# Kernel tuning notes

Hardware: AMD Instinct MI355X
Metric: run time of the kernel (lower is better)

## Reference

```python
import jax, jax.numpy as jnp
import numpy as np

DIM = 256
NUM_HEADS = 8
NUM_NEI = (16, 32)
G = len(NUM_NEI)          # branches
G_H = NUM_HEADS // G      # heads per branch = 4
G_DIM = DIM // G          # channels per branch = 128
HD = G_DIM // G_H         # head dim = 32
SCALE = HD ** (-0.5)
M_MSF = G                 # MSF branches
CHANNEL = DIM // M_MSF    # 128
D_MSF = CHANNEL           # r=1

gelu = lambda t: jax.nn.gelu(t, approximate=False)


def setup_inputs() -> dict:
    key = jax.random.key(0)
    ks = jax.random.split(key, 16)
    B, N = 4, 2048
    s = lambda fan: fan ** (-0.5)
    inp = {
        "x": jax.random.normal(ks[0], (B, N, DIM), jnp.float32),
        "pos": jax.random.uniform(ks[1], (B, N, 3), jnp.float32),
        # qkv linear (no bias); stored as (in, out)
        "Wqkv": jax.random.normal(ks[2], (DIM, 3 * DIM), jnp.float32) * s(DIM),
        # per-branch rel-pos MLPs: Linear(3, g_dim) + GELU
        "Wp0": jax.random.normal(ks[3], (3, G_DIM), jnp.float32) * s(3),
        "bp0": jnp.zeros((G_DIM,), jnp.float32),
        "Wp1": jax.random.normal(ks[4], (3, G_DIM), jnp.float32) * s(3),
        "bp1": jnp.zeros((G_DIM,), jnp.float32),
        # MSF params
        "W_proj": jax.random.normal(ks[5], (DIM, DIM), jnp.float32) * s(DIM),
        "b_proj": jnp.zeros((DIM,), jnp.float32),
        "W_fc1": jax.random.normal(ks[6], (DIM, D_MSF), jnp.float32) * s(DIM),
        "b_fc1": jnp.zeros((D_MSF,), jnp.float32),
        "W_fc2": jax.random.normal(ks[7], (D_MSF, M_MSF * CHANNEL), jnp.float32) * s(D_MSF),
        "b_fc2": jnp.zeros((M_MSF * CHANNEL,), jnp.float32),
        "W_head": jax.random.normal(ks[8], (DIM, DIM), jnp.float32) * s(DIM),
        "b_head": jnp.zeros((DIM,), jnp.float32),
    }
    return inp


def _branch(q, k, v, pos, knn_idx, Wp, bp):
    """One head-group: KNN gather + rel-pos MLP fused attention.
    q,k,v: [B,N,g_dim]; pos: [B,N,3]; knn_idx: [B,N,nk]."""
    B, N, g_dim = k.shape
    nk = knn_idx.shape[-1]
    gather = jax.vmap(lambda t, idx: t[idx])  # per-batch fancy gather -> [B,N,nk,D]
    knn_xyz = gather(pos, knn_idx)                       # [B,N,nk,3]
    kg = gather(k, knn_idx)                              # [B,N,nk,g_dim]
    vg = gather(v, knn_idx)
    # split heads: b n k (h d) -> b h n k d
    split = lambda t: t.reshape(B, N, nk, G_H, HD).transpose(0, 3, 1, 2, 4)
    kg, vg = split(kg), split(vg)
    rel = pos[:, :, None, :] - knn_xyz                   # [B,N,nk,3]
    vrp = split(gelu(rel @ Wp + bp))                     # [B,h,N,nk,d]
    vg = vg + vrp
    attn_rel = vrp.sum(-1)                               # [B,h,N,nk]
    qh = q.reshape(B, N, G_H, HD).transpose(0, 2, 1, 3)  # [B,h,N,d]
    logits = jnp.einsum('bhnd,bhnkd->bhnk', qh, kg) * SCALE + attn_rel
    a = jax.nn.softmax(logits, axis=-1)
    out = jnp.einsum('bhnk,bhnkd->bhnd', a, vg)          # [B,h,N,d]
    return out.transpose(0, 2, 1, 3).reshape(B, N, g_dim)


def _msf(x, W_proj, b_proj, W_fc1, b_fc1, W_fc2, b_fc2, W_head, b_head):
    bs, N, dim = x.shape
    input_groups = x.transpose(0, 2, 1).reshape(bs, M_MSF, CHANNEL, N)
    feats_proj = gelu(x @ W_proj + b_proj)               # [bs,N,dim]
    feats_S = feats_proj.mean(axis=1)                    # global avg pool over N -> [bs,dim]
    feats_Z = gelu(feats_S @ W_fc1 + b_fc1)
    av = (feats_Z @ W_fc2 + b_fc2).reshape(bs, M_MSF, CHANNEL, 1)
    av = jax.nn.softmax(av, axis=1)                      # softmax over branches
    feats_V = (input_groups * av).reshape(bs, dim, N).transpose(0, 2, 1)
    feats_V = feats_V @ W_head + b_head
    return feats_proj + feats_V


def reference(x, pos, Wqkv, Wp0, bp0, Wp1, bp1,
              W_proj, b_proj, W_fc1, b_fc1, W_fc2, b_fc2, W_head, b_head):
    B, N, C = x.shape
    # pairwise squared distances [B,N,N] (broadcast form, as in source)
    dists = jnp.sum((pos[:, :, None, :] - pos[:, None, :, :]) ** 2, axis=-1)
    order = jnp.argsort(dists, axis=-1)                  # [B,N,N]
    qkv = (x @ Wqkv).reshape(B, N, 3, C).transpose(2, 0, 1, 3)  # [3,B,N,C]
    pos_params = [(Wp0, bp0), (Wp1, bp1)]
    outs = []
    for i, nk in enumerate(NUM_NEI):
        sl = slice(i * G_DIM, (i + 1) * G_DIM)
        q, k, v = qkv[0][..., sl], qkv[1][..., sl], qkv[2][..., sl]
        knn_idx = order[:, :, :nk]
        Wp, bp = pos_params[i]
        outs.append(_branch(q, k, v, pos, knn_idx, Wp, bp))
    xcat = jnp.concatenate(outs, axis=-1)                # [B,N,C]
    return _msf(xcat, W_proj, b_proj, W_fc1, b_fc1, W_fc2, b_fc2, W_head, b_head)
```

## Files before the change

kernel.cpp:

```cpp
#include <hip/hip_runtime.h>
#include <cstdint>
#include <cstddef>

#define B_    4
#define NPT   2048
#define DIM_  256
#define QKVW  768
#define XLEN  2097152
#define QLEN  196608
#define PLEN  65536
#define TOTC  (XLEN + QLEN + 2 * PLEN)

typedef unsigned short ushort_t;
typedef unsigned long long u64;
typedef short bf16x8 __attribute__((ext_vector_type(8)));
typedef float f32x4 __attribute__((ext_vector_type(4)));

__device__ __forceinline__ float gelu_f(float x) {
  return 0.5f * x * (1.0f + erff(x * 0.70710678118654752440f));
}

__device__ __forceinline__ float gelu_fast(float x) {
  const float is2 = 0.70710678118654752440f;
  float z = x * is2;
  float az = __builtin_fabsf(z);
  float t = __builtin_amdgcn_rcpf(fmaf(0.3275911f, az, 1.0f));
  float p = fmaf(1.061405429f, t, -1.453152027f);
  p = fmaf(p, t, 1.421413741f);
  p = fmaf(p, t, -0.284496736f);
  p = fmaf(p, t, 0.254829592f);
  p = p * t;
  float e = __expf(-az * az);
  float er = fmaf(-p, e, 1.0f);
  er = __builtin_copysignf(er, x);
  return 0.5f * x * (1.0f + er);
}

__device__ __forceinline__ ushort_t f2bf(float f) {
  unsigned u = __float_as_uint(f);
  unsigned r = (u + 0x7fffu + ((u >> 16) & 1u)) >> 16;
  return (ushort_t)r;
}
__device__ __forceinline__ float bf2f(ushort_t h) {
  return __uint_as_float(((unsigned)h) << 16);
}

template <int CTRL>
__device__ __forceinline__ float dpp_addf(float x) {
  int s = __builtin_amdgcn_update_dpp(0, __float_as_int(x), CTRL, 0xf, 0xf, false);
  return x + __int_as_float(s);
}
template <int CTRL>
__device__ __forceinline__ int dpp_addi(int x) {
  int s = __builtin_amdgcn_update_dpp(0, x, CTRL, 0xf, 0xf, false);
  return x + s;
}
__device__ __forceinline__ float head32_reduce(float u) {
  u = dpp_addf<0x111>(u);
  u = dpp_addf<0x112>(u);
  u = dpp_addf<0x114>(u);
  u = dpp_addf<0x118>(u);
  u = dpp_addf<0x142>(u);
  return u;
}
__device__ __forceinline__ int wave_sum_i(int x) {
  x = dpp_addi<0x111>(x);
  x = dpp_addi<0x112>(x);
  x = dpp_addi<0x114>(x);
  x = dpp_addi<0x118>(x);
  x = dpp_addi<0x142>(x);
  x = dpp_addi<0x143>(x);
  return x;
}

__device__ __forceinline__ bf16x8 scale_bf(bf16x8 v, const float* avk) {
  bf16x8 r;
#pragma unroll
  for (int e = 0; e < 8; e++) {
    float f = bf2f((ushort_t)v[e]) * avk[e];
    r[e] = (short)f2bf(f);
  }
  return r;
}

__global__ __launch_bounds__(256) void convert_kernel(
    const float* __restrict__ x, const float* __restrict__ Wqkv,
    const float* __restrict__ Wproj, const float* __restrict__ Whead,
    ushort_t* __restrict__ xbf, ushort_t* __restrict__ WqkvT,
    ushort_t* __restrict__ WprojT, ushort_t* __restrict__ WheadT,
    float* __restrict__ part) {
  int base = blockIdx.x * 256 + threadIdx.x;
  if (base < 1024) part[base] = 0.f;
  for (int i = base; i < TOTC; i += 2048 * 256) {
    if (i < XLEN) {
      xbf[i] = f2bf(x[i]);
    } else if (i < XLEN + QLEN) {
      int e = i - XLEN;
      int k = e / 768, n = e - k * 768;
      WqkvT[n * 256 + k] = f2bf(Wqkv[e]);
    } else if (i < XLEN + QLEN + PLEN) {
      int e = i - XLEN - QLEN;
      int k = e >> 8, n = e & 255;
      WprojT[n * 256 + k] = f2bf(Wproj[e]);
    } else {
      int e = i - XLEN - QLEN - PLEN;
      int k = e >> 8, n = e & 255;
      WheadT[n * 256 + k] = f2bf(Whead[e]);
    }
  }
}

__global__ __launch_bounds__(64, 4) void knn_gemm0_kernel(
    const float* __restrict__ pos, int* __restrict__ idx_out,
    const ushort_t* __restrict__ A, const ushort_t* __restrict__ BT,
    float* __restrict__ C) {
  __shared__ u64 buf[128];
  __shared__ unsigned cnt;
  int lane = threadIdx.x;
  if (blockIdx.x >= 8192) {
    constexpr int K = 256;
    constexpr int N = 768;
    int quad = lane >> 4, r16 = lane & 15;
    int t0 = blockIdx.x - 8192;
    int m0 = (t0 / 24) * 64, n0 = (t0 % 24) * 32;
    const ushort_t* Ap = A + (size_t)(m0 + r16) * K + quad * 8;
    const ushort_t* Bp = BT + (size_t)(n0 + r16) * K + quad * 8;
    f32x4 acc[4][2] = {};
    bf16x8 af[4], bfv[2], af2[4], bf2[2];
#pragma unroll
    for (int i = 0; i < 4; i++) af[i] = *(const bf16x8*)(Ap + (size_t)i * 16 * K);
#pragma unroll
    for (int j = 0; j < 2; j++) bfv[j] = *(const bf16x8*)(Bp + (size_t)j * 16 * K);
#pragma unroll
    for (int kc = 0; kc < 8; kc++) {
      if (kc < 7) {
        int ko = (kc + 1) * 32;
#pragma unroll
        for (int i = 0; i < 4; i++)
          af2[i] = *(const bf16x8*)(Ap + (size_t)i * 16 * K + ko);
#pragma unroll
        for (int j = 0; j < 2; j++)
          bf2[j] = *(const bf16x8*)(Bp + (size_t)j * 16 * K + ko);
      }
#pragma unroll
      for (int i = 0; i < 4; i++) {
        acc[i][0] = __builtin_amdgcn_mfma_f32_16x16x32_bf16(af[i], bfv[0], acc[i][0], 0, 0, 0);
        acc[i][1] = __builtin_amdgcn_mfma_f32_16x16x32_bf16(af[i], bfv[1], acc[i][1], 0, 0, 0);
      }
#pragma unroll
      for (int i = 0; i < 4; i++) af[i] = af2[i];
      bfv[0] = bf2[0]; bfv[1] = bf2[1];
    }
#pragma unroll
    for (int i = 0; i < 4; i++) {
#pragma unroll
      for (int j = 0; j < 2; j++) {
        int col = n0 + j * 16 + r16;
#pragma unroll
        for (int r = 0; r < 4; r++) {
          int row = m0 + i * 16 + quad * 4 + r;
          C[(size_t)row * N + col] = acc[i][j][r];
        }
      }
    }
    return;
  }
  int wq = blockIdx.x;
  int b = wq >> 11, n = wq & (NPT - 1);
  const float* pb = pos + (size_t)b * NPT * 3;
  float qx = pb[n * 3 + 0], qy = pb[n * 3 + 1], qz = pb[n * 3 + 2];
  u64 keys[32];
  {
#pragma clang fp contract(off)
#pragma unroll
    for (int s = 0; s < 32; s++) {
      int j = lane + (s << 6);
      float dx = qx - pb[j * 3 + 0];
      float dy = qy - pb[j * 3 + 1];
      float dz = qz - pb[j * 3 + 2];
      float d = dx * dx;
      d = d + dy * dy;
      d = d + dz * dz;
      keys[s] = ((u64)__float_as_uint(d) << 32) | (unsigned)j;
    }
  }
  unsigned lo = 0, hi = 0x40400001u;
  for (int it = 0; it < 31 && hi - lo > 1; ++it) {
    unsigned mid = (lo + hi) >> 1;
    int c = 0;
#pragma unroll
    for (int s = 0; s < 32; s++)
      c += ((unsigned)(keys[s] >> 32) < mid) ? 1 : 0;
    c = __builtin_amdgcn_readlane(wave_sum_i(c), 63);
    if (c >= 32) { hi = mid; if (c <= 64) break; }
    else lo = mid;
  }
  unsigned T = hi;
  buf[lane] = ~0ULL;
  buf[lane + 64] = ~0ULL;
  if (lane == 0) cnt = 0;
  __builtin_amdgcn_wave_barrier();
  asm volatile("s_waitcnt lgkmcnt(0)" ::: "memory");
  int cl = 0;
#pragma unroll
  for (int s = 0; s < 32; s++)
    cl += ((unsigned)(keys[s] >> 32) < T) ? 1 : 0;
  unsigned base = atomicAdd(&cnt, (unsigned)cl);
  unsigned w = base;
#pragma unroll
  for (int s = 0; s < 32; s++) {
    if ((unsigned)(keys[s] >> 32) < T && w < 128) {
      buf[w] = keys[s];
      w++;
    }
  }
  __builtin_amdgcn_wave_barrier();
  asm volatile("s_waitcnt lgkmcnt(0)" ::: "memory");
  unsigned total = cnt;
  total = (unsigned)__builtin_amdgcn_readfirstlane((int)total);
  if (total > 128u) total = 128u;
  unsigned mt = (total + 7u) & ~7u;
  u64 k0 = buf[lane];
  u64 k1 = buf[lane + 64];
  int r0 = 0, r1 = 0;
  for (unsigned i = 0; i < mt; i += 8) {
#pragma unroll
    for (int t = 0; t < 8; t++) {
      u64 ki = buf[i + t];
      r0 += (ki < k0) ? 1 : 0;
      r1 += (ki < k1) ? 1 : 0;
    }
  }
  if (r0 < 32) idx_out[(size_t)wq * 32 + r0] = (int)(unsigned)(k0 & 0xffffffffULL);
  if (r1 < 32) idx_out[(size_t)wq * 32 + r1] = (int)(unsigned)(k1 & 0xffffffffULL);
}

template <int MODE>
__global__ __launch_bounds__(64, 4) void gemm_rf(
    const ushort_t* __restrict__ A, const ushort_t* __restrict__ BT,
    const float* __restrict__ bias, const float* __restrict__ extra,
    float* __restrict__ C, float* __restrict__ part,
    const float* __restrict__ av, int N) {
  constexpr int K = 256;
  int lane = threadIdx.x;
  int quad = lane >> 4, r16 = lane & 15;
  int t0 = blockIdx.x;
  int m0 = (t0 >> 3) * 64, n0 = (t0 & 7) * 32;
  int batch = m0 >> 11;
  const ushort_t* Ap = A + (size_t)(m0 + r16) * K + quad * 8;
  const ushort_t* Bp = BT + (size_t)(n0 + r16) * K + quad * 8;
  f32x4 acc[4][2] = {};
  bf16x8 af[4], bf[2], af2[4], bf2[2];
#pragma unroll
  for (int i = 0; i < 4; i++) af[i] = *(const bf16x8*)(Ap + (size_t)i * 16 * K);
#pragma unroll
  for (int j = 0; j < 2; j++) bf[j] = *(const bf16x8*)(Bp + (size_t)j * 16 * K);
#pragma unroll
  for (int kc = 0; kc < 8; kc++) {
    if (kc < 7) {
      int ko = (kc + 1) * 32;
#pragma unroll
      for (int i = 0; i < 4; i++)
        af2[i] = *(const bf16x8*)(Ap + (size_t)i * 16 * K + ko);
#pragma unroll
      for (int j = 0; j < 2; j++)
        bf2[j] = *(const bf16x8*)(Bp + (size_t)j * 16 * K + ko);
    }
    bf16x8 b0 = bf[0], b1 = bf[1];
    if (MODE == 2) {
      const float* avk = av + batch * 256 + kc * 32 + quad * 8;
      b0 = scale_bf(b0, avk);
      b1 = scale_bf(b1, avk);
    }
#pragma unroll
    for (int i = 0; i < 4; i++) {
      acc[i][0] = __builtin_amdgcn_mfma_f32_16x16x32_bf16(af[i], b0, acc[i][0], 0, 0, 0);
      acc[i][1] = __builtin_amdgcn_mfma_f32_16x16x32_bf16(af[i], b1, acc[i][1], 0, 0, 0);
    }
#pragma unroll
    for (int i = 0; i < 4; i++) af[i] = af2[i];
    bf[0] = bf2[0]; bf[1] = bf2[1];
  }
  float cs[2] = {};
#pragma unroll
  for (int i = 0; i < 4; i++) {
#pragma unroll
    for (int j = 0; j < 2; j++) {
      int col = n0 + j * 16 + r16;
#pragma unroll
      for (int r = 0; r < 4; r++) {
        int row = m0 + i * 16 + quad * 4 + r;
        float v = acc[i][j][r];
        if (MODE == 1) { v = gelu_fast(v + bias[col]); cs[j] += v; }
        else if (MODE == 2) v = extra[(size_t)row * 256 + col] + v + bias[col];
        C[(size_t)row * N + col] = v;
      }
    }
  }
  if (MODE == 1) {
#pragma unroll
    for (int j = 0; j < 2; j++) {
      cs[j] += __shfl_xor(cs[j], 16, 64);
      cs[j] += __shfl_xor(cs[j], 32, 64);
    }
    if (quad == 0) {
#pragma unroll
      for (int j = 0; j < 2; j++)
        atomicAdd(&part[batch * 256 + n0 + j * 16 + r16], cs[j]);
    }
  }
}

template <int NK>
__device__ __forceinline__ float attn_loop(
    const float* __restrict__ qkvb, const int* sidx, const float4* srel,
    int g, int c, int lane, float qS, float w0, float w1, float w2, float bb) {
  float den = 0.f, num = 0.f;
#pragma unroll
  for (int j = 0; j < NK; j++) {
    int jj = __builtin_amdgcn_readfirstlane(sidx[j]);
    float4 rr = srel[j];
    const float* kb = qkvb + (size_t)jj * QKVW + 256 + g * 128;
    float kv = kb[c];
    float vv = kb[256 + c];
    float x = fmaf(rr.x, w0, fmaf(rr.y, w1, fmaf(rr.z, w2, bb)));
    float x2 = x * x;
    float z2 = x * fmaf(0.0713548163f, x2, 1.5957691216f);
    float t = __builtin_amdgcn_rcpf(1.0f + __expf(-z2));
    float r = x * t;
    float u = head32_reduce(fmaf(qS, kv, r));
    float l0 = __int_as_float(__builtin_amdgcn_readlane(__float_as_int(u), 31));
    float l1 = __int_as_float(__builtin_amdgcn_readlane(__float_as_int(u), 63));
    float logit = (lane < 32) ? l0 : l1;
    float e = __expf(logit);
    den += e;
    num = fmaf(e, vv + r, num);
  }
  return num * __builtin_amdgcn_rcpf(den);
}

__global__ __launch_bounds__(128) void attn_kernel(
    const float* __restrict__ qkv, const float* __restrict__ pos,
    const int* __restrict__ knn,
    const float* __restrict__ Wp0, const float* __restrict__ bp0,
    const float* __restrict__ Wp1, const float* __restrict__ bp1,
    ushort_t* __restrict__ xcat) {
  const float SCALE = 0.17677669529663687f;
  int u = blockIdx.x;
  int g = blockIdx.y;
  int b = u >> 11, n = u & (NPT - 1);
  int c = threadIdx.x;
  int wave = c >> 6, lane = c & 63;
  __shared__ int s_idx[2][32];
  __shared__ float4 s_rel[2][32];
  const float* qkvb = qkv + (size_t)b * NPT * QKVW;
  if (lane < 32) {
    int j = knn[(size_t)u * 32 + lane];
    s_idx[wave][lane] = j;
    const float* pn = pos + ((size_t)b * NPT + n) * 3;
    const float* pj = pos + ((size_t)b * NPT + j) * 3;
    s_rel[wave][lane] = make_float4(pn[0] - pj[0], pn[1] - pj[1],
                                    pn[2] - pj[2], 0.f);
  }
  __builtin_amdgcn_wave_barrier();
  asm volatile("s_waitcnt lgkmcnt(0)" ::: "memory");
  const float* Wp = g ? Wp1 : Wp0;
  const float* bp = g ? bp1 : bp0;
  float w0 = Wp[c], w1 = Wp[128 + c], w2 = Wp[256 + c], bb = bp[c];
  float qS = qkvb[(size_t)n * QKVW + g * 128 + c] * SCALE;
  float o = (g == 0)
      ? attn_loop<16>(qkvb, s_idx[wave], s_rel[wave], g, c, lane, qS, w0, w1, w2, bb)
      : attn_loop<32>(qkvb, s_idx[wave], s_rel[wave], g, c, lane, qS, w0, w1, w2, bb);
  xcat[((size_t)b * NPT + n) * DIM_ + g * 128 + c] = f2bf(o);
}

__global__ __launch_bounds__(256) void msf_av_kernel(
    const float* __restrict__ part, const float* __restrict__ Wfc1,
    const float* __restrict__ bfc1, const float* __restrict__ Wfc2,
    const float* __restrict__ bfc2, float* __restrict__ av_out) {
  int b = blockIdx.x, t = threadIdx.x;
  __shared__ float S[256], Z[128], A[256];
  S[t] = part[b * 256 + t] * (1.0f / 2048.0f);
  __syncthreads();
  if (t < 128) {
    float z = bfc1[t];
    for (int i = 0; i < 256; i++) z += S[i] * Wfc1[i * 128 + t];
    Z[t] = gelu_f(z);
  }
  __syncthreads();
  float a = bfc2[t];
  for (int j = 0; j < 128; j++) a += Z[j] * Wfc2[j * 256 + t];
  A[t] = a;
  __syncthreads();
  float pA = A[t ^ 128];
  float m = fmaxf(a, pA);
  float e = expf(a - m);
  av_out[b * 256 + t] = e / (e + expf(pA - m));
}

extern "C" void kernel_launch(void* const* d_in, const int* in_sizes, int n_in,
                              void* d_out, int out_size, void* d_ws, size_t ws_size,
                              hipStream_t stream) {
  const float* x     = (const float*)d_in[0];
  const float* pos   = (const float*)d_in[1];
  const float* Wqkv  = (const float*)d_in[2];
  const float* Wp0   = (const float*)d_in[3];
  const float* bp0   = (const float*)d_in[4];
  const float* Wp1   = (const float*)d_in[5];
  const float* bp1   = (const float*)d_in[6];
  const float* Wproj = (const float*)d_in[7];
  const float* bproj = (const float*)d_in[8];
  const float* Wfc1  = (const float*)d_in[9];
  const float* bfc1  = (const float*)d_in[10];
  const float* Wfc2  = (const float*)d_in[11];
  const float* bfc2  = (const float*)d_in[12];
  const float* Whead = (const float*)d_in[13];
  const float* bhead = (const float*)d_in[14];
  float* out = (float*)d_out;

  char* ws = (char*)d_ws;
  size_t off = 0;
  int* idx = (int*)(ws + off);              off += (size_t)B_ * NPT * 32 * 4;
  float* qkv = (float*)(ws + off);          off += (size_t)B_ * NPT * QKVW * 4;
  float* fp = qkv;
  ushort_t* xbf = (ushort_t*)(ws + off);    off += (size_t)B_ * NPT * DIM_ * 2;
  ushort_t* xcat = xbf;
  ushort_t* WqkvT = (ushort_t*)(ws + off);  off += (size_t)QLEN * 2;
  ushort_t* WprojT = (ushort_t*)(ws + off); off += (size_t)PLEN * 2;
  ushort_t* WheadT = (ushort_t*)(ws + off); off += (size_t)PLEN * 2;
  float* part = (float*)(ws + off);         off += 1024 * 4;
  float* av = (float*)(ws + off);           off += 1024 * 4;

  const int M = B_ * NPT;

  convert_kernel<<<2048, 256, 0, stream>>>(x, Wqkv, Wproj, Whead,
                                           xbf, WqkvT, WprojT, WheadT, part);
  knn_gemm0_kernel<<<8192 + 3072, 64, 0, stream>>>(pos, idx, xbf, WqkvT, qkv);
  attn_kernel<<<dim3(M, 2), 128, 0, stream>>>(qkv, pos, idx,
                                              Wp0, bp0, Wp1, bp1, xcat);
  gemm_rf<1><<<1024, 64, 0, stream>>>(xcat, WprojT, bproj, nullptr,
                                      fp, part, nullptr, DIM_);
  msf_av_kernel<<<B_, 256, 0, stream>>>(part, Wfc1, bfc1, Wfc2, bfc2, av);
  gemm_rf<2><<<1024, 64, 0, stream>>>(xcat, WheadT, bhead, fp,
                                      out, nullptr, av, DIM_);
}
```

Baseline: 203.2 us.

## Process two channels per lane in attention kernel with one wave per block

The attention kernel now uses a single 64-lane wave per (point, branch), with each lane handling two adjacent channels through float2 loads. The per-head dot-product reduction becomes a 16-lane ds_swizzle butterfly, since a head of 32 channels now spans 16 lanes. This halves thread count and gather instructions and removes the readlane/select step, at the cost of more work per lane and fewer waves for hiding latency.

```diff
diff --git a/kernel.cpp b/kernel.cpp
--- a/kernel.cpp
+++ b/kernel.cpp
@@ -55,14 +55,6 @@
   int s = __builtin_amdgcn_update_dpp(0, x, CTRL, 0xf, 0xf, false);
   return x + s;
 }
-__device__ __forceinline__ float head32_reduce(float u) {
-  u = dpp_addf<0x111>(u);
-  u = dpp_addf<0x112>(u);
-  u = dpp_addf<0x114>(u);
-  u = dpp_addf<0x118>(u);
-  u = dpp_addf<0x142>(u);
-  return u;
-}
 __device__ __forceinline__ int wave_sum_i(int x) {
   x = dpp_addi<0x111>(x);
   x = dpp_addi<0x112>(x);
@@ -70,6 +62,14 @@
   x = dpp_addi<0x118>(x);
   x = dpp_addi<0x142>(x);
   x = dpp_addi<0x143>(x);
+  return x;
+}
+
+__device__ __forceinline__ float bfly16_sum(float x) {
+  x += __int_as_float(__builtin_amdgcn_ds_swizzle(__float_as_int(x), 0x041F));
+  x += __int_as_float(__builtin_amdgcn_ds_swizzle(__float_as_int(x), 0x081F));
+  x += __int_as_float(__builtin_amdgcn_ds_swizzle(__float_as_int(x), 0x101F));
+  x += __int_as_float(__builtin_amdgcn_ds_swizzle(__float_as_int(x), 0x201F));
   return x;
 }
 
@@ -312,34 +312,34 @@
 }
 
 template <int NK>
-__device__ __forceinline__ float attn_loop(
-    const float* __restrict__ qkvb, const int* sidx, const float4* srel,
-    int g, int c, int lane, float qS, float w0, float w1, float w2, float bb) {
-  float den = 0.f, num = 0.f;
+__device__ __forceinline__ void attn_core(
+    const float* __restrict__ kvbase, int c2, const int* sidx,
+    const float4* srel, float qSx, float qSy,
+    float2 w0, float2 w1, float2 w2, float2 bb,
+    float& num0, float& num1, float& den) {
 #pragma unroll
   for (int j = 0; j < NK; j++) {
     int jj = __builtin_amdgcn_readfirstlane(sidx[j]);
     float4 rr = srel[j];
-    const float* kb = qkvb + (size_t)jj * QKVW + 256 + g * 128;
-    float kv = kb[c];
-    float vv = kb[256 + c];
-    float x = fmaf(rr.x, w0, fmaf(rr.y, w1, fmaf(rr.z, w2, bb)));
-    float x2 = x * x;
-    float z2 = x * fmaf(0.0713548163f, x2, 1.5957691216f);
-    float t = __builtin_amdgcn_rcpf(1.0f + __expf(-z2));
-    float r = x * t;
-    float u = head32_reduce(fmaf(qS, kv, r));
-    float l0 = __int_as_float(__builtin_amdgcn_readlane(__float_as_int(u), 31));
-    float l1 = __int_as_float(__builtin_amdgcn_readlane(__float_as_int(u), 63));
-    float logit = (lane < 32) ? l0 : l1;
+    const float* kb = kvbase + (size_t)jj * QKVW;
+    float2 kv = *(const float2*)(kb + c2);
+    float2 vv = *(const float2*)(kb + 256 + c2);
+    float x0 = fmaf(rr.x, w0.x, fmaf(rr.y, w1.x, fmaf(rr.z, w2.x, bb.x)));
+    float x1 = fmaf(rr.x, w0.y, fmaf(rr.y, w1.y, fmaf(rr.z, w2.y, bb.y)));
+    float z0 = x0 * fmaf(0.0713548163f, x0 * x0, 1.5957691216f);
+    float z1 = x1 * fmaf(0.0713548163f, x1 * x1, 1.5957691216f);
+    float r0 = x0 * __builtin_amdgcn_rcpf(1.0f + __expf(-z0));
+    float r1 = x1 * __builtin_amdgcn_rcpf(1.0f + __expf(-z1));
+    float p = fmaf(qSx, kv.x, r0) + fmaf(qSy, kv.y, r1);
+    float logit = bfly16_sum(p);
     float e = __expf(logit);
     den += e;
-    num = fmaf(e, vv + r, num);
-  }
-  return num * __builtin_amdgcn_rcpf(den);
-}
-
-__global__ __launch_bounds__(128) void attn_kernel(
+    num0 = fmaf(e, vv.x + r0, num0);
+    num1 = fmaf(e, vv.y + r1, num1);
+  }
+}
+
+__global__ __launch_bounds__(64) void attn_kernel(
     const float* __restrict__ qkv, const float* __restrict__ pos,
     const int* __restrict__ knn,
     const float* __restrict__ Wp0, const float* __restrict__ bp0,
@@ -349,29 +349,40 @@
   int u = blockIdx.x;
   int g = blockIdx.y;
   int b = u >> 11, n = u & (NPT - 1);
-  int c = threadIdx.x;
-  int wave = c >> 6, lane = c & 63;
-  __shared__ int s_idx[2][32];
-  __shared__ float4 s_rel[2][32];
+  int lane = threadIdx.x;
+  int c2 = lane * 2;
+  __shared__ int s_idx[32];
+  __shared__ float4 s_rel[32];
   const float* qkvb = qkv + (size_t)b * NPT * QKVW;
   if (lane < 32) {
     int j = knn[(size_t)u * 32 + lane];
-    s_idx[wave][lane] = j;
+    s_idx[lane] = j;
     const float* pn = pos + ((size_t)b * NPT + n) * 3;
     const float* pj = pos + ((size_t)b * NPT + j) * 3;
-    s_rel[wave][lane] = make_float4(pn[0] - pj[0], pn[1] - pj[1],
-                                    pn[2] - pj[2], 0.f);
+    s_rel[lane] = make_float4(pn[0] - pj[0], pn[1] - pj[1],
+                              pn[2] - pj[2], 0.f);
   }
   __builtin_amdgcn_wave_barrier();
   asm volatile("s_waitcnt lgkmcnt(0)" ::: "memory");
   const float* Wp = g ? Wp1 : Wp0;
   const float* bp = g ? bp1 : bp0;
-  float w0 = Wp[c], w1 = Wp[128 + c], w2 = Wp[256 + c], bb = bp[c];
-  float qS = qkvb[(size_t)n * QKVW + g * 128 + c] * SCALE;
-  float o = (g == 0)
-      ? attn_loop<16>(qkvb, s_idx[wave], s_rel[wave], g, c, lane, qS, w0, w1, w2, bb)
-      : attn_loop<32>(qkvb, s_idx[wave], s_rel[wave], g, c, lane, qS, w0, w1, w2, bb);
-  xcat[((size_t)b * NPT + n) * DIM_ + g * 128 + c] = f2bf(o);
+  float2 w0 = *(const float2*)(Wp + c2);
+  float2 w1 = *(const float2*)(Wp + 128 + c2);
+  float2 w2 = *(const float2*)(Wp + 256 + c2);
+  float2 bb = *(const float2*)(bp + c2);
+  float2 q2 = *(const float2*)(qkvb + (size_t)n * QKVW + g * 128 + c2);
+  float qSx = q2.x * SCALE, qSy = q2.y * SCALE;
+  const float* kvbase = qkvb + 256 + g * 128;
+  float num0 = 0.f, num1 = 0.f, den = 0.f;
+  if (g == 0)
+    attn_core<16>(kvbase, c2, s_idx, s_rel, qSx, qSy, w0, w1, w2, bb,
+                  num0, num1, den);
+  else
+    attn_core<32>(kvbase, c2, s_idx, s_rel, qSx, qSy, w0, w1, w2, bb,
+                  num0, num1, den);
+  float inv = __builtin_amdgcn_rcpf(den);
+  unsigned pk = (unsigned)f2bf(num0 * inv) | ((unsigned)f2bf(num1 * inv) << 16);
+  ((unsigned*)xcat)[((size_t)b * NPT + n) * 128 + g * 64 + lane] = pk;
 }
 
 __global__ __launch_bounds__(256) void msf_av_kernel(
@@ -436,8 +447,8 @@
   convert_kernel<<<2048, 256, 0, stream>>>(x, Wqkv, Wproj, Whead,
                                            xbf, WqkvT, WprojT, WheadT, part);
   knn_gemm0_kernel<<<8192 + 3072, 64, 0, stream>>>(pos, idx, xbf, WqkvT, qkv);
-  attn_kernel<<<dim3(M, 2), 128, 0, stream>>>(qkv, pos, idx,
-                                              Wp0, bp0, Wp1, bp1, xcat);
+  attn_kernel<<<dim3(M, 2), 64, 0, stream>>>(qkv, pos, idx,
+                                             Wp0, bp0, Wp1, bp1, xcat);
   gemm_rf<1><<<1024, 64, 0, stream>>>(xcat, WprojT, bproj, nullptr,
                                       fp, part, nullptr, DIM_);
   msf_av_kernel<<<B_, 256, 0, stream>>>(part, Wfc1, bfc1, Wfc2, bfc2, av);
```

Measured after the change: 190.5 us. -6.3%, faster.
